# Optimization experiments

Hardware: AMD Instinct MI355X
Metric: run time of the kernel (lower is better)

The kernel has to match this reference:

```python
import jax, jax.numpy as jnp
import numpy as np

H, W, D = 56, 56, 28            # input_resolution
WS = (7, 7, 7)                  # window size (Wh, Ww, Wd)
SS = (3, 3, 3)                  # shift size
DIM = 96
NH = 3
HD = DIM // NH
N = WS[0] * WS[1] * WS[2]       # 343 tokens per window
NW = (H // WS[0]) * (W // WS[1]) * (D // WS[2])  # 256 windows


def _rel_pos_index():
    Wd, Wh, Ww = WS
    coords = np.stack(np.meshgrid(np.arange(Wd), np.arange(Wh), np.arange(Ww), indexing='ij'))
    cf = coords.reshape(3, -1)
    rel = (cf[:, :, None] - cf[:, None, :]).transpose(1, 2, 0)
    rel[:, :, 0] += Wd - 1
    rel[:, :, 1] += Wh - 1
    rel[:, :, 2] += Ww - 1
    rel[:, :, 0] *= (2 * Wh - 1) * (2 * Ww - 1)
    rel[:, :, 1] *= (2 * Ww - 1)
    return rel.sum(-1)  # (N, N)


def _attn_mask():
    img = np.zeros((H, W, D), np.float32)
    def slices(w, s):
        return (slice(0, -w), slice(-w, -s), slice(-s, None))
    cnt = 0
    for hs in slices(WS[0], SS[0]):
        for ws in slices(WS[1], SS[1]):
            for ds in slices(WS[2], SS[2]):
                img[hs, ws, ds] = cnt
                cnt += 1
    mw = img.reshape(H // WS[0], WS[0], W // WS[1], WS[1], D // WS[2], WS[2])
    mw = mw.transpose(0, 2, 4, 1, 3, 5).reshape(-1, N)  # (NW, N)
    am = mw[:, None, :] - mw[:, :, None]
    return np.where(am != 0, np.float32(-100.0), np.float32(0.0))


REL_IDX = jnp.asarray(_rel_pos_index())
ATTN_MASK = jnp.asarray(_attn_mask())  # (NW, N, N)


def _ln(x, g, b, eps=1e-5):
    m = x.mean(-1, keepdims=True)
    v = jnp.mean((x - m) ** 2, -1, keepdims=True)
    return (x - m) * jax.lax.rsqrt(v + eps) * g + b


def _forward(x, n1g, n1b, qkv_w, qkv_b, rpb, proj_w, proj_b,
             n2g, n2b, fc1_w, fc1_b, fc2_w, fc2_b):
    B, L, C = x.shape
    shortcut = x
    h = _ln(x, n1g, n1b).reshape(B, H, W, D, C)
    # cyclic shift
    h = jnp.roll(h, (-SS[0], -SS[1], -SS[2]), axis=(1, 2, 3))
    # window partition -> (B*NW, N, C)
    h = h.reshape(B, H // WS[0], WS[0], W // WS[1], WS[1], D // WS[2], WS[2], C)
    h = h.transpose(0, 1, 3, 5, 2, 4, 6, 7).reshape(-1, N, C)
    # qkv
    qkv = (h @ qkv_w + qkv_b).reshape(-1, N, 3, NH, HD).transpose(2, 0, 3, 1, 4)
    q, k, v = qkv[0] * (HD ** -0.5), qkv[1], qkv[2]  # (B*NW, NH, N, HD)
    attn = jnp.einsum('bhnd,bhmd->bhnm', q, k)
    bias = rpb[REL_IDX.reshape(-1)].reshape(N, N, NH).transpose(2, 0, 1)
    attn = attn + bias[None]
    # shifted-window mask
    attn = attn.reshape(B, NW, NH, N, N) + ATTN_MASK[None, :, None]
    attn = jax.nn.softmax(attn.reshape(-1, NH, N, N), axis=-1)
    o = jnp.einsum('bhnm,bhmd->bhnd', attn, v).transpose(0, 2, 1, 3).reshape(-1, N, C)
    o = o @ proj_w + proj_b
    # window reverse
    o = o.reshape(B, H // WS[0], W // WS[1], D // WS[2], WS[0], WS[1], WS[2], C)
    o = o.transpose(0, 1, 4, 2, 5, 3, 6, 7).reshape(B, H, W, D, C)
    o = jnp.roll(o, SS, axis=(1, 2, 3)).reshape(B, L, C)
    x = shortcut + o
    h2 = _ln(x, n2g, n2b)
    h2 = jax.nn.gelu(h2 @ fc1_w + fc1_b, approximate=False) @ fc2_w + fc2_b
    return x + h2


def setup_inputs() -> dict:
    key = jax.random.key(0)
    ks = jax.random.split(key, 6)
    C, FF = DIM, 4 * DIM
    f32 = jnp.float32
    return {
        'x': jax.random.normal(ks[0], (1, H * W * D, C), f32),
        'n1g': jnp.ones((C,), f32), 'n1b': jnp.zeros((C,), f32),
        'qkv_w': jax.random.normal(ks[1], (C, 3 * C), f32) * 0.02,
        'qkv_b': jnp.zeros((3 * C,), f32),
        'rpb': jax.random.normal(ks[2], ((2 * WS[0] - 1) * (2 * WS[1] - 1) * (2 * WS[2] - 1), NH), f32) * 0.02,
        'proj_w': jax.random.normal(ks[3], (C, C), f32) * 0.02,
        'proj_b': jnp.zeros((C,), f32),
        'n2g': jnp.ones((C,), f32), 'n2b': jnp.zeros((C,), f32),
        'fc1_w': jax.random.normal(ks[4], (C, FF), f32) * 0.02,
        'fc1_b': jnp.zeros((FF,), f32),
        'fc2_w': jax.random.normal(ks[5], (FF, C), f32) * 0.02,
        'fc2_b': jnp.zeros((C,), f32),
    }


def reference(x, n1g, n1b, qkv_w, qkv_b, rpb, proj_w, proj_b,
              n2g, n2b, fc1_w, fc1_b, fc2_w, fc2_b):
    return _forward(x, n1g, n1b, qkv_w, qkv_b, rpb, proj_w, proj_b,
                    n2g, n2b, fc1_w, fc1_b, fc2_w, fc2_b)
```

## Files before the change

### kernel.cpp

```cpp
#include <hip/hip_runtime.h>
#include <hip/hip_bf16.h>


#define L_TOK 87808

typedef unsigned int uint;
typedef __attribute__((ext_vector_type(8))) short short8;
typedef __attribute__((ext_vector_type(4))) float f32x4;

__device__ __forceinline__ float bflo(uint u){ union{uint x; float f;} a; a.x = u << 16; return a.f; }
__device__ __forceinline__ float bfhi(uint u){ union{uint x; float f;} a; a.x = u & 0xffff0000u; return a.f; }
__device__ __forceinline__ float bfval(unsigned short w){ union{uint x; float f;} a; a.x = (uint)w << 16; return a.f; }
__device__ __forceinline__ unsigned short f2bfbits(float f){
  union{float f; uint u;} a; a.f = f;
  uint u = a.u;
  u += 0x7fffu + ((u >> 16) & 1u);
  return (unsigned short)(u >> 16);
}
__device__ __forceinline__ unsigned short bfb(float f){
  __hip_bfloat16 h = __float2bfloat16(f);
  return *reinterpret_cast<unsigned short*>(&h);
}
__device__ __forceinline__ uint pkbf(float a, float b){
  return ((uint)bfb(b) << 16) | (uint)bfb(a);
}
__device__ __forceinline__ uint pack2(float a, float b){
  return ((uint)f2bfbits(b) << 16) | (uint)f2bfbits(a);
}
__device__ __forceinline__ uint4 pack8(const float* p){
  uint4 u;
  u.x = pack2(p[0], p[1]); u.y = pack2(p[2], p[3]);
  u.z = pack2(p[4], p[5]); u.w = pack2(p[6], p[7]);
  return u;
}
__device__ __forceinline__ uint4 pack8g(const float* gp){
  float t[8];
  *(float4*)&t[0] = *(const float4*)gp;
  *(float4*)&t[4] = *(const float4*)(gp + 4);
  return pack8(t);
}

__global__ __launch_bounds__(256)
void k_tr(const float* __restrict__ src, unsigned short* __restrict__ dst,
          int K, int N)
{
  const int idx = blockIdx.x * 256 + threadIdx.x;
  if (idx < K * N) {
    const int n = idx / K, k = idx % K;
    dst[idx] = f2bfbits(src[(size_t)k * N + n]);
  }
}

__global__ __launch_bounds__(256)
void k_mb(const float* __restrict__ rpbg, unsigned short* __restrict__ MB)
{
  const int idx = blockIdx.x * 256 + threadIdx.x;
  const int cls = idx / (3*352*352);
  const int rem = idx - cls * (3*352*352);
  const int h = rem / (352*352);
  const int rem2 = rem - h * (352*352);
  const int q = rem2 / 352;
  const int k = rem2 - q * 352;
  unsigned short v = 0xFF80;
  if (q < 343 && k < 343) {
    const int q0 = q/49, q1 = (q%49)/7, q2 = q%7;
    const int k0 = k/49, k1 = (k%49)/7, k2 = k%7;
    const int bq = q0*169 + q1*13 + q2;
    const int bk = k0*169 + k1*13 + k2;
    float bias = rpbg[(size_t)(bq - bk + 1098)*3 + h];
    int cq = 0, ck = 0;
    if (cls & 4) { cq += ((q0 < 4) ? 1 : 2)*9; ck += ((k0 < 4) ? 1 : 2)*9; }
    if (cls & 2) { cq += ((q1 < 4) ? 1 : 2)*3; ck += ((k1 < 4) ? 1 : 2)*3; }
    if (cls & 1) { cq += (q2 < 4) ? 1 : 2;     ck += (k2 < 4) ? 1 : 2; }
    if (cq != ck) bias -= 100.0f;
    v = f2bfbits(bias);
  }
  MB[idx] = v;
}

__global__ __launch_bounds__(256)
void k_qkv_ln(const float* __restrict__ x,
              const float* __restrict__ n1g,
              const float* __restrict__ n1b,
              const unsigned short* __restrict__ qkvwt,
              const float* __restrict__ bias, size_t headStride,
              __hip_bfloat16* __restrict__ qb,
              __hip_bfloat16* __restrict__ kb,
              __hip_bfloat16* __restrict__ vb)
{
  __shared__ __align__(16) unsigned short As[64][104];
  __shared__ uint srcOff[64];
  __shared__ float gLds[96], bLds[96];
  __shared__ float pSum[256], pSq[256];
  __shared__ float mLds[64], sLds[64];

  const int tid = threadIdx.x;
  const int wave = tid >> 6, lane = tid & 63;
  const int row0 = blockIdx.x * 64;
  const int h = (int)blockIdx.y;
  __hip_bfloat16* qh = qb + (size_t)h * headStride;
  __hip_bfloat16* kh = kb + (size_t)h * headStride;
  __hip_bfloat16* vh = vb + (size_t)h * headStride;

  if (tid < 64) {
    const uint row = (uint)(row0 + tid);
    const uint win = row / 343u, n = row % 343u;
    const uint wh = win >> 5, ww = (win >> 2) & 7u, wd = win & 3u;
    const uint ih = n / 49u, rr = n % 49u, iw = rr / 7u, id = rr % 7u;
    uint gh = wh*7u + ih + 3u; if (gh >= 56u) gh -= 56u;
    uint gw = ww*7u + iw + 3u; if (gw >= 56u) gw -= 56u;
    uint gd = wd*7u + id + 3u; if (gd >= 28u) gd -= 28u;
    srcOff[tid] = ((gh*56u + gw)*28u + gd) * 96u;
  }
  if (tid < 96) { gLds[tid] = n1g[tid]; bLds[tid] = n1b[tid]; }
  __syncthreads();

  for (int i = tid; i < 768; i += 256) {
    const int r = i / 12, kk = (i % 12) * 8;
    *(uint4*)&As[r][kk] = pack8g(x + srcOff[r] + kk);
  }
  __syncthreads();

  {
    const int r = tid & 63, seg = tid >> 6;
    float s = 0.0f, sq = 0.0f;
    #pragma unroll
    for (int j = 0; j < 24; ++j) {
      const float v = bfval(As[r][seg*24 + j]);
      s += v; sq += v*v;
    }
    pSum[tid] = s; pSq[tid] = sq;
  }
  __syncthreads();
  if (tid < 64) {
    const float s  = pSum[tid] + pSum[tid+64] + pSum[tid+128] + pSum[tid+192];
    const float sq = pSq[tid] + pSq[tid+64] + pSq[tid+128] + pSq[tid+192];
    const float mean = s * (1.0f/96.0f);
    mLds[tid] = mean;
    sLds[tid] = rsqrtf(sq*(1.0f/96.0f) - mean*mean + 1e-5f);
  }
  __syncthreads();
  for (int i = tid; i < 768; i += 256) {
    const int r = i / 12, kk = (i % 12) * 8;
    uint4 u = *(uint4*)&As[r][kk];
    const float m = mLds[r], sc = sLds[r];
    float v[8];
    v[0]=bflo(u.x); v[1]=bfhi(u.x); v[2]=bflo(u.y); v[3]=bfhi(u.y);
    v[4]=bflo(u.z); v[5]=bfhi(u.z); v[6]=bflo(u.w); v[7]=bfhi(u.w);
    #pragma unroll
    for (int j = 0; j < 8; ++j) v[j] = (v[j] - m)*sc*gLds[kk+j] + bLds[kk+j];
    *(uint4*)&As[r][kk] = pack8(v);
  }
  __syncthreads();

  f32x4 acc[6];
  #pragma unroll
  for (int i = 0; i < 6; ++i) acc[i] = (f32x4){0.f, 0.f, 0.f, 0.f};
  const int ml = lane & 15, q8 = (lane >> 4) * 8;
  #pragma unroll
  for (int kc = 0; kc < 3; ++kc) {
    const short8 a = *(const short8*)&As[wave*16 + ml][kc*32 + q8];
    #pragma unroll
    for (int nt = 0; nt < 6; ++nt) {
      const int col = nt*16 + ml;
      const int wcol = (col >> 5)*96 + h*32 + (col & 31);
      const short8 b = *(const short8*)(qkvwt + (size_t)wcol*96 + kc*32 + q8);
      acc[nt] = __builtin_amdgcn_mfma_f32_16x16x32_bf16(a, b, acc[nt], 0, 0, 0);
    }
  }

  const float qscale = 0.17677669529663687f;
  #pragma unroll
  for (int r = 0; r < 4; ++r) {
    const size_t row = (size_t)(row0 + wave*16 + (lane >> 4)*4 + r);
    #pragma unroll
    for (int nt = 0; nt < 6; ++nt) {
      const int col = nt*16 + ml;
      const int part = col >> 5, d = col & 31;
      float v = acc[nt][r] + bias[part*96 + h*32 + d];
      if (part == 0) v *= qscale;
      __hip_bfloat16* dst = (part == 0) ? qh : ((part == 1) ? kh : vh);
      dst[row*32 + d] = __float2bfloat16(v);
    }
  }
}

__global__ __launch_bounds__(256, 4)
void k_attn_v10(const __hip_bfloat16* __restrict__ qg,
                const __hip_bfloat16* __restrict__ kg,
                const __hip_bfloat16* __restrict__ vg,
                size_t headStride,
                const unsigned short* __restrict__ MB,
                float* __restrict__ ob)
{
  __shared__ __align__(16) unsigned short vt[32*344 + 16];
  __shared__ __align__(16) unsigned short Pc[4][16*56];
  __shared__ float lred[4][16];

  const int tid = threadIdx.x;
  const int wave = tid >> 6, lane = tid & 63;
  const uint win = blockIdx.x;
  const int hh = (int)blockIdx.y;
  const int mtBase = (int)blockIdx.z * 11;
  const size_t wbase = (size_t)hh * headStride + (size_t)win * (343*32);
  const unsigned short* qw = (const unsigned short*)qg + wbase;
  const unsigned short* kw = (const unsigned short*)kg + wbase;
  const unsigned short* vw = (const unsigned short*)vg + wbase;

  const uint wh = win >> 5, ww = (win >> 2) & 7u, wd = win & 3u;
  const int cls = ((wh == 7u) ? 4 : 0) | ((ww == 7u) ? 2 : 0) | ((wd == 3u) ? 1 : 0);
  const unsigned short* MBh = MB + ((size_t)cls*3 + hh) * (352*352);

  for (int t = tid; t < 343; t += 256) {
    const uint4* src = (const uint4*)(vw + (size_t)t*32);
    #pragma unroll
    for (int c4 = 0; c4 < 4; ++c4) {
      const uint4 u = src[c4];
      const int d = c4*8;
      vt[(d+0)*344 + t] = (unsigned short)(u.x & 0xffffu);
      vt[(d+1)*344 + t] = (unsigned short)(u.x >> 16);
      vt[(d+2)*344 + t] = (unsigned short)(u.y & 0xffffu);
      vt[(d+3)*344 + t] = (unsigned short)(u.y >> 16);
      vt[(d+4)*344 + t] = (unsigned short)(u.z & 0xffffu);
      vt[(d+5)*344 + t] = (unsigned short)(u.z >> 16);
      vt[(d+6)*344 + t] = (unsigned short)(u.w & 0xffffu);
      vt[(d+7)*344 + t] = (unsigned short)(u.w >> 16);
    }
  }
  if (tid < 32) vt[tid*344 + 343] = 0;
  if (tid < 16) vt[32*344 + tid] = 0;
  __syncthreads();

  const int ml = lane & 15, g = lane >> 4, g8 = g*8;
  unsigned short* Pw = &Pc[wave][0];

  for (int mt = mtBase + wave; mt < mtBase + 11; mt += 4) {
    const int q = mt*16 + ml;
    const short8 qf = *(const short8*)(qw + (size_t)q*32 + g8);
    const unsigned short* MBq = MBh + (size_t)q * 352;
    float l = 0.0f;
    f32x4 o0 = {0.f,0.f,0.f,0.f}, o1 = {0.f,0.f,0.f,0.f};

    for (int kc = 0; kc < 11; ++kc) {
      const short8 kf0 = *(const short8*)(kw + (size_t)(kc*32 + ml)*32 + g8);
      const short8 kf1 = *(const short8*)(kw + (size_t)(kc*32 + 16 + ml)*32 + g8);
      f32x4 s0 = __builtin_amdgcn_mfma_f32_16x16x32_bf16(kf0, qf, (f32x4){0.f,0.f,0.f,0.f}, 0, 0, 0);
      f32x4 s1 = __builtin_amdgcn_mfma_f32_16x16x32_bf16(kf1, qf, (f32x4){0.f,0.f,0.f,0.f}, 0, 0, 0);

      const ushort4 u0 = *(const ushort4*)(MBq + kc*32 + 4*g);
      const ushort4 u1 = *(const ushort4*)(MBq + kc*32 + 16 + 4*g);

      float p0 = __expf(s0[0] + bfval(u0.x));
      float p1 = __expf(s0[1] + bfval(u0.y));
      float p2 = __expf(s0[2] + bfval(u0.z));
      float p3 = __expf(s0[3] + bfval(u0.w));
      float p4 = __expf(s1[0] + bfval(u1.x));
      float p5 = __expf(s1[1] + bfval(u1.y));
      float p6 = __expf(s1[2] + bfval(u1.z));
      float p7 = __expf(s1[3] + bfval(u1.w));
      l += ((p0 + p1) + (p2 + p3)) + ((p4 + p5) + (p6 + p7));

      uint2 wlo, whi;
      wlo.x = pkbf(p0, p1); wlo.y = pkbf(p2, p3);
      whi.x = pkbf(p4, p5); whi.y = pkbf(p6, p7);
      *(uint2*)&Pw[ml*56 + 4*g]      = wlo;
      *(uint2*)&Pw[ml*56 + 16 + 4*g] = whi;

      const short8 pf  = *(const short8*)&Pw[ml*56 + g8];
      const short8 vf0 = *(const short8*)&vt[(size_t)ml*344 + kc*32 + g8];
      const short8 vf1 = *(const short8*)&vt[(size_t)(16 + ml)*344 + kc*32 + g8];
      o0 = __builtin_amdgcn_mfma_f32_16x16x32_bf16(pf, vf0, o0, 0, 0, 0);
      o1 = __builtin_amdgcn_mfma_f32_16x16x32_bf16(pf, vf1, o1, 0, 0, 0);
    }

    l += __shfl_xor(l, 16);
    l += __shfl_xor(l, 32);
    if (g == 0) lred[wave][ml] = 1.0f / l;
    const float4 li = *(const float4*)&lred[wave][4*g];
    #pragma unroll
    for (int r = 0; r < 4; ++r) {
      const int row = mt*16 + 4*g + r;
      if (row < 343) {
        float* op = ob + ((size_t)win*343 + (uint)row)*96 + hh*32;
        op[ml]      = o0[r] * li[r];
        op[16 + ml] = o1[r] * li[r];
      }
    }
  }
}

__global__ __launch_bounds__(256, 4)
void k_attn_v9(const __hip_bfloat16* __restrict__ qg,
               const __hip_bfloat16* __restrict__ kg,
               const __hip_bfloat16* __restrict__ vg,
               size_t headStride,
               const float* __restrict__ rpbg,
               float* __restrict__ ob)
{
  __shared__ __align__(16) unsigned short vt[32*344 + 16];
  __shared__ __align__(16) unsigned short Pc[4][16*40];
  __shared__ short baseT[352];
  __shared__ unsigned char cntT[352];
  __shared__ unsigned short rpB[2197];

  const int tid = threadIdx.x;
  const int wave = tid >> 6, lane = tid & 63;
  const uint win = blockIdx.x;
  const int hh = (int)blockIdx.y;
  const int mtBase = (int)blockIdx.z * 11;
  const size_t wbase = (size_t)hh * headStride + (size_t)win * (343*32);
  const unsigned short* qw = (const unsigned short*)qg + wbase;
  const unsigned short* kw = (const unsigned short*)kg + wbase;
  const unsigned short* vw = (const unsigned short*)vg + wbase;

  for (int i = tid; i < 2197; i += 256) rpB[i] = f2bfbits(rpbg[i*3 + hh]);
  const uint wh = win >> 5, ww = (win >> 2) & 7u, wd = win & 3u;
  for (int i = tid; i < 352; i += 256) {
    if (i < 343) {
      const uint c0 = (uint)i/49u, rr = (uint)i%49u, c1 = rr/7u, c2 = rr%7u;
      baseT[i] = (short)(c0*169u + c1*13u + c2);
      const uint g0 = wh*7u + c0, g1 = ww*7u + c1, g2 = wd*7u + c2;
      const uint rh = (g0 < 49u) ? 0u : ((g0 < 53u) ? 1u : 2u);
      const uint rw = (g1 < 49u) ? 0u : ((g1 < 53u) ? 1u : 2u);
      const uint rd = (g2 < 21u) ? 0u : ((g2 < 25u) ? 1u : 2u);
      cntT[i] = (unsigned char)(rh*9u + rw*3u + rd);
    } else { baseT[i] = 0; cntT[i] = 255; }
  }
  for (int t = tid; t < 343; t += 256) {
    const uint4* src = (const uint4*)(vw + (size_t)t*32);
    #pragma unroll
    for (int c4 = 0; c4 < 4; ++c4) {
      const uint4 u = src[c4];
      const int d = c4*8;
      vt[(d+0)*344 + t] = (unsigned short)(u.x & 0xffffu);
      vt[(d+1)*344 + t] = (unsigned short)(u.x >> 16);
      vt[(d+2)*344 + t] = (unsigned short)(u.y & 0xffffu);
      vt[(d+3)*344 + t] = (unsigned short)(u.y >> 16);
      vt[(d+4)*344 + t] = (unsigned short)(u.z & 0xffffu);
      vt[(d+5)*344 + t] = (unsigned short)(u.z >> 16);
      vt[(d+6)*344 + t] = (unsigned short)(u.w & 0xffffu);
      vt[(d+7)*344 + t] = (unsigned short)(u.w >> 16);
    }
  }
  if (tid < 32) vt[tid*344 + 343] = 0;
  if (tid < 16) vt[32*344 + tid] = 0;
  __syncthreads();

  const int ml = lane & 15, g = lane >> 4, g8 = g*8;
  unsigned short* Pw = &Pc[wave][0];

  for (int mt = mtBase + wave; mt < mtBase + 11; mt += 4) {
    const int qrow = mt*16;
    const short8 qf = *(const short8*)(qw + (size_t)(qrow + ml)*32 + g8);
    int cnR[4], biR[4];
    #pragma unroll
    for (int r = 0; r < 4; ++r) {
      const int gi = qrow + g*4 + r;
      cnR[r] = (int)cntT[gi];
      biR[r] = (int)baseT[gi] + 1098;
    }
    float m_[4], l_[4];
    #pragma unroll
    for (int r = 0; r < 4; ++r) { m_[r] = -1e30f; l_[r] = 0.0f; }
    f32x4 o0 = {0.f,0.f,0.f,0.f}, o1 = {0.f,0.f,0.f,0.f};

    for (int kc = 0; kc < 11; ++kc) {
      const int c0 = kc*32 + ml, c1 = c0 + 16;
      const short8 kf0 = *(const short8*)(kw + (size_t)c0*32 + g8);
      const short8 kf1 = *(const short8*)(kw + (size_t)c1*32 + g8);
      f32x4 s0 = __builtin_amdgcn_mfma_f32_16x16x32_bf16(qf, kf0, (f32x4){0.f,0.f,0.f,0.f}, 0, 0, 0);
      f32x4 s1 = __builtin_amdgcn_mfma_f32_16x16x32_bf16(qf, kf1, (f32x4){0.f,0.f,0.f,0.f}, 0, 0, 0);

      float bv0[4], bv1[4];
      const int bj0 = (int)baseT[c0], bj1 = (int)baseT[c1];
      #pragma unroll
      for (int r = 0; r < 4; ++r) {
        bv0[r] = bfval(rpB[biR[r] - bj0]);
        bv1[r] = bfval(rpB[biR[r] - bj1]);
      }
      const int cj0 = (int)cntT[c0], cj1 = (int)cntT[c1];

      float a_[4];
      #pragma unroll
      for (int r = 0; r < 4; ++r) {
        float v0 = s0[r] + bv0[r];
        float v1 = s1[r] + bv1[r];
        v0 += (cj0 == cnR[r]) ? 0.0f : -100.0f;
        v1 += (cj1 == cnR[r]) ? 0.0f : -100.0f;
        v1 = (c1 < 343) ? v1 : -1e30f;
        s0[r] = v0; s1[r] = v1;
        float cm = fmaxf(v0, v1);
        cm = fmaxf(cm, __shfl_xor(cm, 1));
        cm = fmaxf(cm, __shfl_xor(cm, 2));
        cm = fmaxf(cm, __shfl_xor(cm, 4));
        cm = fmaxf(cm, __shfl_xor(cm, 8));
        const float mn = fmaxf(m_[r], cm);
        a_[r] = __expf(m_[r] - mn);
        m_[r] = mn;
      }
      #pragma unroll
      for (int r = 0; r < 4; ++r) {
        const float p0 = __expf(s0[r] - m_[r]);
        const float p1 = __expf(s1[r] - m_[r]);
        Pw[(g*4 + r)*40 + ml]      = f2bfbits(p0);
        Pw[(g*4 + r)*40 + 16 + ml] = f2bfbits(p1);
        float cs = p0 + p1;
        cs += __shfl_xor(cs, 1);
        cs += __shfl_xor(cs, 2);
        cs += __shfl_xor(cs, 4);
        cs += __shfl_xor(cs, 8);
        l_[r] = l_[r]*a_[r] + cs;
        o0[r] *= a_[r];
        o1[r] *= a_[r];
      }
      const short8 pf  = *(const short8*)&Pw[ml*40 + g8];
      const short8 vf0 = *(const short8*)&vt[(size_t)ml*344 + kc*32 + g8];
      const short8 vf1 = *(const short8*)&vt[(size_t)(16 + ml)*344 + kc*32 + g8];
      o0 = __builtin_amdgcn_mfma_f32_16x16x32_bf16(pf, vf0, o0, 0, 0, 0);
      o1 = __builtin_amdgcn_mfma_f32_16x16x32_bf16(pf, vf1, o1, 0, 0, 0);
    }

    #pragma unroll
    for (int r = 0; r < 4; ++r) {
      const int row = qrow + g*4 + r;
      if (row < 343) {
        const float inv = 1.0f / l_[r];
        float* op = ob + ((size_t)win*343 + (uint)row)*96 + hh*32;
        op[ml]      = o0[r] * inv;
        op[16 + ml] = o1[r] * inv;
      }
    }
  }
}

__global__ __launch_bounds__(256)
void k_proj(const float* __restrict__ A,
            const unsigned short* __restrict__ pwt,
            const float* __restrict__ bias,
            const float* __restrict__ xin,
            __hip_bfloat16* __restrict__ xres)
{
  __shared__ __align__(16) unsigned short As[64][104];
  const int tid = threadIdx.x;
  const int wave = tid >> 6, lane = tid & 63;
  const int row0 = blockIdx.x * 64;

  for (int i = tid; i < 768; i += 256) {
    const int r = i / 12, kk = (i % 12) * 8;
    *(uint4*)&As[r][kk] = pack8g(A + (size_t)(row0 + r)*96 + kk);
  }
  __syncthreads();

  f32x4 acc[6];
  #pragma unroll
  for (int i = 0; i < 6; ++i) acc[i] = (f32x4){0.f, 0.f, 0.f, 0.f};
  const int ml = lane & 15, q8 = (lane >> 4) * 8;
  #pragma unroll
  for (int kc = 0; kc < 3; ++kc) {
    const short8 a = *(const short8*)&As[wave*16 + ml][kc*32 + q8];
    #pragma unroll
    for (int nt = 0; nt < 6; ++nt) {
      const short8 b = *(const short8*)(pwt + (size_t)(nt*16 + ml)*96 + kc*32 + q8);
      acc[nt] = __builtin_amdgcn_mfma_f32_16x16x32_bf16(a, b, acc[nt], 0, 0, 0);
    }
  }

  #pragma unroll
  for (int r = 0; r < 4; ++r) {
    const uint row = (uint)(row0 + wave*16 + (lane >> 4)*4 + r);
    const uint win = row / 343u, n = row % 343u;
    const uint wh = win >> 5, ww = (win >> 2) & 7u, wd = win & 3u;
    const uint ih = n / 49u, rr = n % 49u, iw = rr / 7u, id = rr % 7u;
    uint gh = wh*7u + ih + 3u; if (gh >= 56u) gh -= 56u;
    uint gw = ww*7u + iw + 3u; if (gw >= 56u) gw -= 56u;
    uint gd = wd*7u + id + 3u; if (gd >= 28u) gd -= 28u;
    const size_t gt = (size_t)((gh*56u + gw)*28u + gd) * 96;
    #pragma unroll
    for (int nt = 0; nt < 6; ++nt) {
      const int col = nt*16 + ml;
      xres[gt + col] = __float2bfloat16(acc[nt][r] + bias[col] + xin[gt + col]);
    }
  }
}

__global__ __launch_bounds__(256, 2)
void k_mlp(const __hip_bfloat16* __restrict__ xresb,
           const float* __restrict__ n2g,
           const float* __restrict__ n2b,
           const unsigned short* __restrict__ w1t,
           const float* __restrict__ b1,
           const unsigned short* __restrict__ w2t,
           const float* __restrict__ b2,
           float* __restrict__ out)
{
  __shared__ __align__(16) unsigned short As[64][104];
  __shared__ __align__(16) unsigned short inter[64][392];
  float* scr  = (float*)&inter[0][0];
  float* pSum = scr;
  float* pSq  = scr + 256;
  float* gL   = scr + 512;
  float* bL   = scr + 608;
  float* mL   = scr + 704;
  float* sL   = scr + 768;

  const int tid = threadIdx.x;
  const int wave = tid >> 6, lane = tid & 63;
  const int row0 = blockIdx.x * 64;
  const int ml = lane & 15, g = lane >> 4, g8 = g*8;

  if (tid < 96) { gL[tid] = n2g[tid]; bL[tid] = n2b[tid]; }
  for (int i = tid; i < 768; i += 256) {
    const int r = i / 12, kk = (i % 12) * 8;
    *(uint4*)&As[r][kk] = *(const uint4*)(xresb + (size_t)(row0 + r)*96 + kk);
  }
  __syncthreads();

  {
    const int r = tid & 63, seg = tid >> 6;
    float s = 0.0f, sq = 0.0f;
    #pragma unroll
    for (int j3 = 0; j3 < 3; ++j3) {
      const uint4 u = *(const uint4*)&As[r][seg*24 + j3*8];
      float v[8];
      v[0]=bflo(u.x); v[1]=bfhi(u.x); v[2]=bflo(u.y); v[3]=bfhi(u.y);
      v[4]=bflo(u.z); v[5]=bfhi(u.z); v[6]=bflo(u.w); v[7]=bfhi(u.w);
      #pragma unroll
      for (int j = 0; j < 8; ++j) { s += v[j]; sq += v[j]*v[j]; }
    }
    pSum[tid] = s; pSq[tid] = sq;
  }
  __syncthreads();
  if (tid < 64) {
    const float s  = pSum[tid] + pSum[tid+64] + pSum[tid+128] + pSum[tid+192];
    const float sq = pSq[tid] + pSq[tid+64] + pSq[tid+128] + pSq[tid+192];
    const float mean = s * (1.0f/96.0f);
    mL[tid] = mean;
    sL[tid] = rsqrtf(sq*(1.0f/96.0f) - mean*mean + 1e-5f);
  }
  __syncthreads();
  for (int i = tid; i < 768; i += 256) {
    const int r = i / 12, kk = (i % 12) * 8;
    uint4 u = *(uint4*)&As[r][kk];
    const float m = mL[r], sc = sL[r];
    float v[8];
    v[0]=bflo(u.x); v[1]=bfhi(u.x); v[2]=bflo(u.y); v[3]=bfhi(u.y);
    v[4]=bflo(u.z); v[5]=bfhi(u.z); v[6]=bflo(u.w); v[7]=bfhi(u.w);
    #pragma unroll
    for (int j = 0; j < 8; ++j) v[j] = (v[j] - m)*sc*gL[kk+j] + bL[kk+j];
    *(uint4*)&As[r][kk] = pack8(v);
  }
  __syncthreads();

  short8 af[4][3];
  #pragma unroll
  for (int mt = 0; mt < 4; ++mt)
    #pragma unroll
    for (int kc = 0; kc < 3; ++kc)
      af[mt][kc] = *(const short8*)&As[mt*16 + ml][kc*32 + g8];

  const int nb = 96 * wave;
  #pragma unroll
  for (int ny = 0; ny < 2; ++ny) {
    short8 bf[3][3];
    #pragma unroll
    for (int nt = 0; nt < 3; ++nt)
      #pragma unroll
      for (int kc = 0; kc < 3; ++kc)
        bf[nt][kc] = *(const short8*)(w1t + (size_t)(nb + 48*ny + 16*nt + ml)*96 + kc*32 + g8);

    f32x4 acc[4][3];
    #pragma unroll
    for (int mt = 0; mt < 4; ++mt)
      #pragma unroll
      for (int nt = 0; nt < 3; ++nt)
        acc[mt][nt] = (f32x4){0.f, 0.f, 0.f, 0.f};

    #pragma unroll
    for (int kc = 0; kc < 3; ++kc)
      #pragma unroll
      for (int nt = 0; nt < 3; ++nt)
        #pragma unroll
        for (int mt = 0; mt < 4; ++mt)
          acc[mt][nt] = __builtin_amdgcn_mfma_f32_16x16x32_bf16(af[mt][kc], bf[nt][kc], acc[mt][nt], 0, 0, 0);

    #pragma unroll
    for (int nt = 0; nt < 3; ++nt) {
      const int col = nb + 48*ny + 16*nt + ml;
      const float b1v = b1[col];
      #pragma unroll
      for (int mt = 0; mt < 4; ++mt) {
        #pragma unroll
        for (int r = 0; r < 4; ++r) {
          float v = acc[mt][nt][r] + b1v;
          v = 0.5f * v * (1.0f + erff(v * 0.70710678118654752f));
          inter[mt*16 + 4*g + r][col] = f2bfbits(v);
        }
      }
    }
  }
  __syncthreads();

  const int rb = 32 * (wave >> 1);
  const int cb = 48 * (wave & 1);
  f32x4 acc2[2][3];
  #pragma unroll
  for (int i = 0; i < 2; ++i)
    #pragma unroll
    for (int nt = 0; nt < 3; ++nt)
      acc2[i][nt] = (f32x4){0.f, 0.f, 0.f, 0.f};

  #pragma unroll
  for (int kc = 0; kc < 12; ++kc) {
    short8 a0 = *(const short8*)&inter[rb + ml][kc*32 + g8];
    short8 a1 = *(const short8*)&inter[rb + 16 + ml][kc*32 + g8];
    #pragma unroll
    for (int nt = 0; nt < 3; ++nt) {
      const short8 b = *(const short8*)(w2t + (size_t)(cb + 16*nt + ml)*384 + kc*32 + g8);
      acc2[0][nt] = __builtin_amdgcn_mfma_f32_16x16x32_bf16(a0, b, acc2[0][nt], 0, 0, 0);
      acc2[1][nt] = __builtin_amdgcn_mfma_f32_16x16x32_bf16(a1, b, acc2[1][nt], 0, 0, 0);
    }
  }

  const unsigned short* xu = (const unsigned short*)xresb;
  #pragma unroll
  for (int i = 0; i < 2; ++i) {
    #pragma unroll
    for (int nt = 0; nt < 3; ++nt) {
      const int col = cb + 16*nt + ml;
      const float b2v = b2[col];
      #pragma unroll
      for (int r = 0; r < 4; ++r) {
        const size_t row = (size_t)(row0 + rb + 16*i + 4*g + r);
        out[row*96 + col] = acc2[i][nt][r] + b2v + bfval(xu[row*96 + col]);
      }
    }
  }
}

extern "C" void kernel_launch(void* const* d_in, const int* in_sizes, int n_in,
                              void* d_out, int out_size, void* d_ws, size_t ws_size,
                              hipStream_t stream)
{
  (void)in_sizes; (void)n_in; (void)out_size;
  const float* x    = (const float*)d_in[0];
  const float* n1g  = (const float*)d_in[1];
  const float* n1b  = (const float*)d_in[2];
  const float* qkvw = (const float*)d_in[3];
  const float* qkvb = (const float*)d_in[4];
  const float* rpb  = (const float*)d_in[5];
  const float* pw   = (const float*)d_in[6];
  const float* pb   = (const float*)d_in[7];
  const float* n2g  = (const float*)d_in[8];
  const float* n2b  = (const float*)d_in[9];
  const float* f1w  = (const float*)d_in[10];
  const float* f1b  = (const float*)d_in[11];
  const float* f2w  = (const float*)d_in[12];
  const float* f2b  = (const float*)d_in[13];
  float* out = (float*)d_out;

  const size_t E = (size_t)L_TOK * 96;
  __hip_bfloat16* qb = (__hip_bfloat16*)d_ws;
  __hip_bfloat16* kb = qb + E;
  __hip_bfloat16* vb = kb + E;
  __hip_bfloat16* xres = (__hip_bfloat16*)d_ws;
  float* ob = out;
  const size_t hs = (size_t)L_TOK * 32;

  unsigned short* qkvwt = (unsigned short*)d_out;
  unsigned short* pwt   = (unsigned short*)kb;
  unsigned short* w1t   = pwt + 9216;
  unsigned short* w2t   = w1t + 36864;

  const size_t MB_BYTES = (size_t)8 * 3 * 352 * 352 * 2;
  unsigned short* MBp = nullptr;
  if (ws_size >= (size_t)6 * E + MB_BYTES) {
    MBp = (unsigned short*)((char*)d_ws + (size_t)6 * E);
    k_mb<<<11616, 256, 0, stream>>>(rpb, MBp);
  }

  k_tr<<<108, 256, 0, stream>>>(qkvw, qkvwt, 96, 288);
  k_qkv_ln<<<dim3(L_TOK/64, 3), 256, 0, stream>>>(
      x, n1g, n1b, qkvwt, qkvb, hs, qb, kb, vb);
  if (MBp)
    k_attn_v10<<<dim3(256, 3, 2), 256, 0, stream>>>(qb, kb, vb, hs, MBp, ob);
  else
    k_attn_v9<<<dim3(256, 3, 2), 256, 0, stream>>>(qb, kb, vb, hs, rpb, ob);
  k_tr<<<36, 256, 0, stream>>>(pw, pwt, 96, 96);
  k_tr<<<144, 256, 0, stream>>>(f1w, w1t, 96, 384);
  k_tr<<<144, 256, 0, stream>>>(f2w, w2t, 384, 96);
  k_proj<<<L_TOK/64, 256, 0, stream>>>(ob, pwt, pb, x, xres);
  k_mlp<<<L_TOK/64, 256, 0, stream>>>(xres, n2g, n2b, w1t, f1b, w2t, f2b, out);
}
```

Before: 294.9 us.

## Fuse QKV heads into one block, tile proj by 128 rows, split MLP hidden

The QKV+LayerNorm kernel now computes all three heads in one block instead of launching one block per head, so LayerNorm and the gathered input load are done once per 64 rows rather than three times. The projection kernel processes 128 rows per block, reusing the weight fragments across two M tiles. The MLP kernel splits the 384-wide hidden layer into two halves to shrink its LDS buffer, which allows a higher occupancy bound of 4. It also replaces erff with an Abramowitz-Stegun polynomial GELU, which is slightly less accurate and adds an extra barrier.

New measurement: 294.6 us. No clear change (-0.1%).

```diff
diff --git a/kernel.cpp b/kernel.cpp
--- a/kernel.cpp
+++ b/kernel.cpp
@@ -38,6 +38,15 @@
   *(float4*)&t[0] = *(const float4*)gp;
   *(float4*)&t[4] = *(const float4*)(gp + 4);
   return pack8(t);
+}
+__device__ __forceinline__ float gelu_f(float v){
+  const float ax = fabsf(v) * 0.70710678118654752f;
+  const float t  = 1.0f / (1.0f + 0.3275911f * ax);
+  const float poly = t*(0.254829592f + t*(-0.284496736f + t*(1.421413741f +
+                     t*(-1.453152027f + t*1.061405429f))));
+  float erfv = 1.0f - poly * __expf(-ax*ax);
+  erfv = copysignf(erfv, v);
+  return 0.5f * v * (1.0f + erfv);
 }
 
 __global__ __launch_bounds__(256)
@@ -97,10 +106,6 @@
   const int tid = threadIdx.x;
   const int wave = tid >> 6, lane = tid & 63;
   const int row0 = blockIdx.x * 64;
-  const int h = (int)blockIdx.y;
-  __hip_bfloat16* qh = qb + (size_t)h * headStride;
-  __hip_bfloat16* kh = kb + (size_t)h * headStride;
-  __hip_bfloat16* vh = vb + (size_t)h * headStride;
 
   if (tid < 64) {
     const uint row = (uint)(row0 + tid);
@@ -125,9 +130,13 @@
     const int r = tid & 63, seg = tid >> 6;
     float s = 0.0f, sq = 0.0f;
     #pragma unroll
-    for (int j = 0; j < 24; ++j) {
-      const float v = bfval(As[r][seg*24 + j]);
-      s += v; sq += v*v;
+    for (int j3 = 0; j3 < 3; ++j3) {
+      const uint4 u = *(const uint4*)&As[r][seg*24 + j3*8];
+      float v[8];
+      v[0]=bflo(u.x); v[1]=bfhi(u.x); v[2]=bflo(u.y); v[3]=bfhi(u.y);
+      v[4]=bflo(u.z); v[5]=bfhi(u.z); v[6]=bflo(u.w); v[7]=bfhi(u.w);
+      #pragma unroll
+      for (int j = 0; j < 8; ++j) { s += v[j]; sq += v[j]*v[j]; }
     }
     pSum[tid] = s; pSq[tid] = sq;
   }
@@ -153,34 +162,37 @@
   }
   __syncthreads();
 
-  f32x4 acc[6];
-  #pragma unroll
-  for (int i = 0; i < 6; ++i) acc[i] = (f32x4){0.f, 0.f, 0.f, 0.f};
+  f32x4 acc[18];
+  #pragma unroll
+  for (int i = 0; i < 18; ++i) acc[i] = (f32x4){0.f, 0.f, 0.f, 0.f};
   const int ml = lane & 15, q8 = (lane >> 4) * 8;
   #pragma unroll
   for (int kc = 0; kc < 3; ++kc) {
     const short8 a = *(const short8*)&As[wave*16 + ml][kc*32 + q8];
     #pragma unroll
-    for (int nt = 0; nt < 6; ++nt) {
-      const int col = nt*16 + ml;
-      const int wcol = (col >> 5)*96 + h*32 + (col & 31);
-      const short8 b = *(const short8*)(qkvwt + (size_t)wcol*96 + kc*32 + q8);
+    for (int nt = 0; nt < 18; ++nt) {
+      const short8 b = *(const short8*)(qkvwt + (size_t)(nt*16 + ml)*96 + kc*32 + q8);
       acc[nt] = __builtin_amdgcn_mfma_f32_16x16x32_bf16(a, b, acc[nt], 0, 0, 0);
     }
   }
 
   const float qscale = 0.17677669529663687f;
   #pragma unroll
-  for (int r = 0; r < 4; ++r) {
-    const size_t row = (size_t)(row0 + wave*16 + (lane >> 4)*4 + r);
-    #pragma unroll
-    for (int nt = 0; nt < 6; ++nt) {
-      const int col = nt*16 + ml;
-      const int part = col >> 5, d = col & 31;
-      float v = acc[nt][r] + bias[part*96 + h*32 + d];
+  for (int nt = 0; nt < 18; ++nt) {
+    const int nbase = nt * 16;
+    const int part = nbase / 96;
+    const int rem  = nbase - part * 96;
+    const int h    = rem >> 5;
+    const int dbase= rem & 31;
+    __hip_bfloat16* base = (part == 0) ? qb : ((part == 1) ? kb : vb);
+    __hip_bfloat16* dst = base + (size_t)h * headStride;
+    const float bv = bias[nbase + ml];
+    #pragma unroll
+    for (int r = 0; r < 4; ++r) {
+      const size_t row = (size_t)(row0 + wave*16 + (lane >> 4)*4 + r);
+      float v = acc[nt][r] + bv;
       if (part == 0) v *= qscale;
-      __hip_bfloat16* dst = (part == 0) ? qh : ((part == 1) ? kh : vh);
-      dst[row*32 + d] = __float2bfloat16(v);
+      dst[row*32 + dbase + ml] = __float2bfloat16(v);
     }
   }
 }
@@ -440,50 +452,57 @@
             const float* __restrict__ xin,
             __hip_bfloat16* __restrict__ xres)
 {
-  __shared__ __align__(16) unsigned short As[64][104];
+  __shared__ __align__(16) unsigned short As[128][104];
   const int tid = threadIdx.x;
   const int wave = tid >> 6, lane = tid & 63;
-  const int row0 = blockIdx.x * 64;
-
-  for (int i = tid; i < 768; i += 256) {
+  const int row0 = blockIdx.x * 128;
+
+  for (int i = tid; i < 1536; i += 256) {
     const int r = i / 12, kk = (i % 12) * 8;
     *(uint4*)&As[r][kk] = pack8g(A + (size_t)(row0 + r)*96 + kk);
   }
   __syncthreads();
 
-  f32x4 acc[6];
-  #pragma unroll
-  for (int i = 0; i < 6; ++i) acc[i] = (f32x4){0.f, 0.f, 0.f, 0.f};
+  f32x4 acc[2][6];
+  #pragma unroll
+  for (int mt = 0; mt < 2; ++mt)
+    #pragma unroll
+    for (int i = 0; i < 6; ++i) acc[mt][i] = (f32x4){0.f, 0.f, 0.f, 0.f};
   const int ml = lane & 15, q8 = (lane >> 4) * 8;
   #pragma unroll
   for (int kc = 0; kc < 3; ++kc) {
-    const short8 a = *(const short8*)&As[wave*16 + ml][kc*32 + q8];
+    const short8 a0 = *(const short8*)&As[wave*32 + ml][kc*32 + q8];
+    const short8 a1 = *(const short8*)&As[wave*32 + 16 + ml][kc*32 + q8];
     #pragma unroll
     for (int nt = 0; nt < 6; ++nt) {
       const short8 b = *(const short8*)(pwt + (size_t)(nt*16 + ml)*96 + kc*32 + q8);
-      acc[nt] = __builtin_amdgcn_mfma_f32_16x16x32_bf16(a, b, acc[nt], 0, 0, 0);
-    }
-  }
-
-  #pragma unroll
-  for (int r = 0; r < 4; ++r) {
-    const uint row = (uint)(row0 + wave*16 + (lane >> 4)*4 + r);
-    const uint win = row / 343u, n = row % 343u;
-    const uint wh = win >> 5, ww = (win >> 2) & 7u, wd = win & 3u;
-    const uint ih = n / 49u, rr = n % 49u, iw = rr / 7u, id = rr % 7u;
-    uint gh = wh*7u + ih + 3u; if (gh >= 56u) gh -= 56u;
-    uint gw = ww*7u + iw + 3u; if (gw >= 56u) gw -= 56u;
-    uint gd = wd*7u + id + 3u; if (gd >= 28u) gd -= 28u;
-    const size_t gt = (size_t)((gh*56u + gw)*28u + gd) * 96;
-    #pragma unroll
-    for (int nt = 0; nt < 6; ++nt) {
-      const int col = nt*16 + ml;
-      xres[gt + col] = __float2bfloat16(acc[nt][r] + bias[col] + xin[gt + col]);
-    }
-  }
-}
-
-__global__ __launch_bounds__(256, 2)
+      acc[0][nt] = __builtin_amdgcn_mfma_f32_16x16x32_bf16(a0, b, acc[0][nt], 0, 0, 0);
+      acc[1][nt] = __builtin_amdgcn_mfma_f32_16x16x32_bf16(a1, b, acc[1][nt], 0, 0, 0);
+    }
+  }
+
+  #pragma unroll
+  for (int mt = 0; mt < 2; ++mt) {
+    #pragma unroll
+    for (int r = 0; r < 4; ++r) {
+      const uint row = (uint)(row0 + wave*32 + mt*16 + (lane >> 4)*4 + r);
+      const uint win = row / 343u, n = row % 343u;
+      const uint wh = win >> 5, ww = (win >> 2) & 7u, wd = win & 3u;
+      const uint ih = n / 49u, rr = n % 49u, iw = rr / 7u, id = rr % 7u;
+      uint gh = wh*7u + ih + 3u; if (gh >= 56u) gh -= 56u;
+      uint gw = ww*7u + iw + 3u; if (gw >= 56u) gw -= 56u;
+      uint gd = wd*7u + id + 3u; if (gd >= 28u) gd -= 28u;
+      const size_t gt = (size_t)((gh*56u + gw)*28u + gd) * 96;
+      #pragma unroll
+      for (int nt = 0; nt < 6; ++nt) {
+        const int col = nt*16 + ml;
+        xres[gt + col] = __float2bfloat16(acc[mt][nt][r] + bias[col] + xin[gt + col]);
+      }
+    }
+  }
+}
+
+__global__ __launch_bounds__(256, 4)
 void k_mlp(const __hip_bfloat16* __restrict__ xresb,
            const float* __restrict__ n2g,
            const float* __restrict__ n2b,
@@ -494,7 +513,7 @@
            float* __restrict__ out)
 {
   __shared__ __align__(16) unsigned short As[64][104];
-  __shared__ __align__(16) unsigned short inter[64][392];
+  __shared__ __align__(16) unsigned short inter[64][200];
   float* scr  = (float*)&inter[0][0];
   float* pSum = scr;
   float* pSq  = scr + 256;
@@ -558,15 +577,27 @@
     for (int kc = 0; kc < 3; ++kc)
       af[mt][kc] = *(const short8*)&As[mt*16 + ml][kc*32 + g8];
 
-  const int nb = 96 * wave;
-  #pragma unroll
-  for (int ny = 0; ny < 2; ++ny) {
+  const int rb = 32 * (wave >> 1);
+  const int cb = 48 * (wave & 1);
+  f32x4 acc2[2][3];
+  #pragma unroll
+  for (int i = 0; i < 2; ++i)
+    #pragma unroll
+    for (int nt = 0; nt < 3; ++nt)
+      acc2[i][nt] = (f32x4){0.f, 0.f, 0.f, 0.f};
+
+  #pragma unroll
+  for (int H = 0; H < 2; ++H) {
+    if (H) __syncthreads();
+
+    const int nbg = H*192 + 48*wave;
+    const int cl0 = 48*wave;
     short8 bf[3][3];
     #pragma unroll
     for (int nt = 0; nt < 3; ++nt)
       #pragma unroll
       for (int kc = 0; kc < 3; ++kc)
-        bf[nt][kc] = *(const short8*)(w1t + (size_t)(nb + 48*ny + 16*nt + ml)*96 + kc*32 + g8);
+        bf[nt][kc] = *(const short8*)(w1t + (size_t)(nbg + 16*nt + ml)*96 + kc*32 + g8);
 
     f32x4 acc[4][3];
     #pragma unroll
@@ -585,39 +616,28 @@
 
     #pragma unroll
     for (int nt = 0; nt < 3; ++nt) {
-      const int col = nb + 48*ny + 16*nt + ml;
-      const float b1v = b1[col];
+      const float b1v = b1[nbg + 16*nt + ml];
+      const int c = cl0 + 16*nt + ml;
       #pragma unroll
       for (int mt = 0; mt < 4; ++mt) {
         #pragma unroll
         for (int r = 0; r < 4; ++r) {
-          float v = acc[mt][nt][r] + b1v;
-          v = 0.5f * v * (1.0f + erff(v * 0.70710678118654752f));
-          inter[mt*16 + 4*g + r][col] = f2bfbits(v);
+          inter[mt*16 + 4*g + r][c] = f2bfbits(gelu_f(acc[mt][nt][r] + b1v));
         }
       }
     }
-  }
-  __syncthreads();
-
-  const int rb = 32 * (wave >> 1);
-  const int cb = 48 * (wave & 1);
-  f32x4 acc2[2][3];
-  #pragma unroll
-  for (int i = 0; i < 2; ++i)
-    #pragma unroll
-    for (int nt = 0; nt < 3; ++nt)
-      acc2[i][nt] = (f32x4){0.f, 0.f, 0.f, 0.f};
-
-  #pragma unroll
-  for (int kc = 0; kc < 12; ++kc) {
-    short8 a0 = *(const short8*)&inter[rb + ml][kc*32 + g8];
-    short8 a1 = *(const short8*)&inter[rb + 16 + ml][kc*32 + g8];
-    #pragma unroll
-    for (int nt = 0; nt < 3; ++nt) {
-      const short8 b = *(const short8*)(w2t + (size_t)(cb + 16*nt + ml)*384 + kc*32 + g8);
-      acc2[0][nt] = __builtin_amdgcn_mfma_f32_16x16x32_bf16(a0, b, acc2[0][nt], 0, 0, 0);
-      acc2[1][nt] = __builtin_amdgcn_mfma_f32_16x16x32_bf16(a1, b, acc2[1][nt], 0, 0, 0);
+    __syncthreads();
+
+    #pragma unroll
+    for (int kcl = 0; kcl < 6; ++kcl) {
+      const short8 a0 = *(const short8*)&inter[rb + ml][kcl*32 + g8];
+      const short8 a1 = *(const short8*)&inter[rb + 16 + ml][kcl*32 + g8];
+      #pragma unroll
+      for (int nt = 0; nt < 3; ++nt) {
+        const short8 b = *(const short8*)(w2t + (size_t)(cb + 16*nt + ml)*384 + H*192 + kcl*32 + g8);
+        acc2[0][nt] = __builtin_amdgcn_mfma_f32_16x16x32_bf16(a0, b, acc2[0][nt], 0, 0, 0);
+        acc2[1][nt] = __builtin_amdgcn_mfma_f32_16x16x32_bf16(a1, b, acc2[1][nt], 0, 0, 0);
+      }
     }
   }
 
@@ -679,7 +699,7 @@
   }
 
   k_tr<<<108, 256, 0, stream>>>(qkvw, qkvwt, 96, 288);
-  k_qkv_ln<<<dim3(L_TOK/64, 3), 256, 0, stream>>>(
+  k_qkv_ln<<<L_TOK/64, 256, 0, stream>>>(
       x, n1g, n1b, qkvwt, qkvb, hs, qb, kb, vb);
   if (MBp)
     k_attn_v10<<<dim3(256, 3, 2), 256, 0, stream>>>(qb, kb, vb, hs, MBp, ob);
@@ -688,6 +708,6 @@
   k_tr<<<36, 256, 0, stream>>>(pw, pwt, 96, 96);
   k_tr<<<144, 256, 0, stream>>>(f1w, w1t, 96, 384);
   k_tr<<<144, 256, 0, stream>>>(f2w, w2t, 384, 96);
-  k_proj<<<L_TOK/64, 256, 0, stream>>>(ob, pwt, pb, x, xres);
+  k_proj<<<L_TOK/128, 256, 0, stream>>>(ob, pwt, pb, x, xres);
   k_mlp<<<L_TOK/64, 256, 0, stream>>>(xres, n2g, n2b, w1t, f1b, w2t, f2b, out);
 }
```
